# Kernel tuning notes

Measured on AMD Instinct MI355X. Metric: run time of the kernel, lower is better.

## Reference

```python
import jax, jax.numpy as jnp
import numpy as np
from jax import lax

K = 3      # kernel size
PAD = 1    # padding (stride=1, dilation=1, single offset group)


def _deform_conv2d(x, off, weight, bias):
    # x: [B,C,H,W], off: [B,2*K*K,H,W] (y,x per tap), weight: [O,C,K,K], bias: [O]
    B, C, H, W = x.shape
    KK = K * K
    off = off.reshape(B, KK, 2, H, W)
    off_y, off_x = off[:, :, 0], off[:, :, 1]          # [B,KK,H,W]

    kh = jnp.repeat(jnp.arange(K, dtype=x.dtype), K)   # [KK] tap row offsets
    kw = jnp.tile(jnp.arange(K, dtype=x.dtype), K)     # [KK] tap col offsets
    py = (jnp.arange(H, dtype=x.dtype)[None, None, :, None] - PAD
          + kh[None, :, None, None] + off_y)           # [B,KK,H,W] sample rows
    px = (jnp.arange(W, dtype=x.dtype)[None, None, None, :] - PAD
          + kw[None, :, None, None] + off_x)           # [B,KK,H,W] sample cols

    y0 = jnp.floor(py); x0 = jnp.floor(px)
    wy1 = py - y0; wx1 = px - x0
    wy0 = 1.0 - wy1; wx0 = 1.0 - wx1

    bidx = jnp.arange(B)[:, None, None, None]

    def gather(iy, ix):
        # zero outside the input (torchvision semantics)
        valid = (iy >= 0) & (iy < H) & (ix >= 0) & (ix < W)
        iyc = jnp.clip(iy, 0, H - 1).astype(jnp.int32)
        ixc = jnp.clip(ix, 0, W - 1).astype(jnp.int32)
        v = x[bidx, :, iyc, ixc]                       # [B,KK,H,W,C]
        return v * valid[..., None].astype(x.dtype)

    samp = (gather(y0, x0)           * (wy0 * wx0)[..., None]
            + gather(y0, x0 + 1)     * (wy0 * wx1)[..., None]
            + gather(y0 + 1, x0)     * (wy1 * wx0)[..., None]
            + gather(y0 + 1, x0 + 1) * (wy1 * wx1)[..., None])  # [B,KK,H,W,C]

    w = weight.reshape(weight.shape[0], C, KK)          # [O,C,KK]
    out = jnp.einsum('bkhwc,ock->bohw', samp, w) + bias[None, :, None, None]
    return out


def setup_inputs() -> dict:
    key = jax.random.key(0)
    k1, k2, k3 = jax.random.split(key, 3)
    B, C, O, H, W = 4, 64, 64, 128, 128
    x = jax.random.normal(k1, (B, C, H, W), dtype=jnp.float32)
    offset_w = jax.random.normal(k2, (2 * K * K, C, 3, 3), dtype=jnp.float32) * 0.02
    offset_b = jnp.zeros((2 * K * K,), dtype=jnp.float32)
    weight = jax.random.normal(k3, (O, C, K, K), dtype=jnp.float32) * 0.01
    bias = jnp.zeros((O,), dtype=jnp.float32)
    return {"x": x, "offset_w": offset_w, "offset_b": offset_b,
            "weight": weight, "bias": bias}


def reference(x, offset_w, offset_b, weight, bias):
    # offset-predicting conv (3x3, pad 1)
    off = lax.conv_general_dilated(
        x, offset_w, window_strides=(1, 1), padding='SAME',
        dimension_numbers=('NCHW', 'OIHW', 'NCHW')) + offset_b[None, :, None, None]
    return _deform_conv2d(x, off, weight, bias)
```

## Files before the change

kernel.cpp:

```cpp
#include <hip/hip_runtime.h>
#include <hip/hip_bf16.h>


typedef short short8 __attribute__((ext_vector_type(8)));
typedef short short4v __attribute__((ext_vector_type(4)));
typedef float f32x4 __attribute__((ext_vector_type(4)));

static __device__ inline short bf16s(float f) {
    __hip_bfloat16 h = __float2bfloat16(f);
    return *(short*)&h;
}
static __device__ inline float lo2f(unsigned u) { return __uint_as_float(u << 16); }
static __device__ inline float hi2f(unsigned u) { return __uint_as_float(u & 0xffff0000u); }

__global__ void prep_kernel(const float* __restrict__ offset_w,
                            const float* __restrict__ weight,
                            __hip_bfloat16* __restrict__ Wb,
                            __hip_bfloat16* __restrict__ OWb)
{
    int id = blockIdx.x * 256 + threadIdx.x;
    if (id < 36864) {
        int j    = id & 7;
        int lane = (id >> 3) & 63;
        int id3  = id >> 9;
        int s    = id3 % 18;
        int otile = id3 / 18;
        int n = lane & 15, q = lane >> 4;
        int kap = s * 32 + q * 8 + j;
        int k = kap >> 6, c = kap & 63;
        int o = otile * 16 + n;
        Wb[id] = __float2bfloat16(weight[(o * 64 + c) * 9 + k]);
    }
    int id2 = id - 36864;
    if (id2 >= 0 && id2 < 18432) {
        int j    = id2 & 7;
        int lane = (id2 >> 3) & 63;
        int id3  = id2 >> 9;
        int s    = id3 % 18;
        int ntile = id3 / 18;
        int n = lane & 15, q = lane >> 4;
        int kap = s * 32 + q * 8 + j;
        int k = kap >> 6, c = kap & 63;
        int o = ntile * 16 + n;
        float v = (o < 18) ? offset_w[(o * 64 + c) * 9 + k] : 0.0f;
        OWb[id2] = __float2bfloat16(v);
    }
}

__global__ void transpose_kernel(const float* __restrict__ x, __hip_bfloat16* __restrict__ xB)
{
    __shared__ __align__(16) float lds[128 * 65];
    int bh = blockIdx.x;
    int b = bh >> 7, h = bh & 127;
    int t = threadIdx.x;
    int w = t & 127, chalf = t >> 7;
    for (int i = 0; i < 32; ++i) {
        int c = i * 2 + chalf;
        lds[w * 65 + c] = x[((b * 64 + c) * 128 + h) * 128 + w];
    }
    __syncthreads();
    unsigned* dst = (unsigned*)(xB + ((b * 128 + h) * 128) * 64);
    for (int i = 0; i < 16; ++i) {
        int L = i * 256 + t;
        int ww = L >> 5, c2 = L & 31;
        float f0 = lds[ww * 65 + c2 * 2];
        float f1 = lds[ww * 65 + c2 * 2 + 1];
        unsigned pk = ((unsigned)bf16s(f0) & 0xffffu) | ((unsigned)bf16s(f1) << 16);
        dst[L] = pk;
    }
}

__global__ __launch_bounds__(256, 6) void deform_kernel(
    const __hip_bfloat16* __restrict__ xB,
    const __hip_bfloat16* __restrict__ Wb,
    const __hip_bfloat16* __restrict__ OWb,
    const float* __restrict__ offset_b,
    const float* __restrict__ bias,
    float* __restrict__ out)
{
    __shared__ __align__(16) short sampB[18 * 16 * 40];
    __shared__ __align__(16) float offL[288];

    int t = threadIdx.x, wv = t >> 6, lane = t & 63;
    int bid = blockIdx.x;
    int b  = bid >> 10;
    int h  = (bid >> 3) & 127;
    int w0 = (bid & 7) << 4;

    short* patch = sampB;

    {
        int c2 = t & 31, pg = t >> 5;
        const __hip_bfloat16* xbb = xB + b * (128 * 128 * 64) + c2 * 2;
#pragma unroll
        for (int i = 0; i < 7; ++i) {
            int pix = i * 8 + pg;
            if (pix < 54) {
                int row = pix / 18, col = pix - row * 18;
                int hh = h - 1 + row, ww2 = w0 - 1 + col;
                unsigned v = 0;
                if (hh >= 0 && hh < 128 && ww2 >= 0 && ww2 < 128)
                    v = *(const unsigned*)(xbb + (hh * 128 + ww2) * 64);
                *(unsigned*)&patch[pix * 80 + c2 * 2] = v;
            }
        }
    }
    __syncthreads();

    if (wv < 2) {
        int n = lane & 15, q = lane >> 4;
        const short8* Bw = (const short8*)OWb + (wv * 18) * 64 + lane;
        f32x4 acc = {0.f, 0.f, 0.f, 0.f};
#pragma unroll
        for (int s = 0; s < 18; ++s) {
            int k = s >> 1;
            int ky = k / 3, kx = k - ky * 3;
            int pix = ky * 18 + n + kx;
            const short8 a = *(const short8*)&patch[pix * 80 + (s & 1) * 32 + q * 8];
            acc = __builtin_amdgcn_mfma_f32_16x16x32_bf16(a, Bw[s * 64], acc, 0, 0, 0);
        }
        int o = wv * 16 + n;
        if (o < 18) {
            float bo = offset_b[o];
#pragma unroll
            for (int r = 0; r < 4; ++r)
                offL[o * 16 + q * 4 + r] = acc[r] + bo;
        }
    }
    __syncthreads();

    {
        int g = lane >> 4, c4 = lane & 15;
        int p = wv * 4 + g;
        const __hip_bfloat16* xb4 = xB + b * (128 * 128 * 64) + c4 * 4;

        float offy[9], offx[9];
#pragma unroll
        for (int k = 0; k < 9; ++k) {
            offy[k] = offL[(2 * k) * 16 + p];
            offx[k] = offL[(2 * k + 1) * 16 + p];
        }

#pragma unroll
        for (int k = 0; k < 9; ++k) {
            float py = (float)(h - 1 + (k / 3)) + offy[k];
            float px = (float)(w0 + p - 1 + (k % 3)) + offx[k];
            float y0f = floorf(py), x0f = floorf(px);
            float wy1 = py - y0f, wx1 = px - x0f;
            float wy0 = 1.0f - wy1, wx0 = 1.0f - wx1;
            int iy = (int)y0f, ix = (int)x0f;
            bool y0v = (iy >= 0) && (iy < 128);
            bool y1v = (iy >= -1) && (iy < 127);
            bool x0v = (ix >= 0) && (ix < 128);
            bool x1v = (ix >= -1) && (ix < 127);
            int iy0c = min(max(iy, 0), 127), iy1c = min(max(iy + 1, 0), 127);
            int ix0c = min(max(ix, 0), 127), ix1c = min(max(ix + 1, 0), 127);
            int e00 = (iy0c * 128 + ix0c) * 64;
            int e01 = (iy0c * 128 + ix1c) * 64;
            int e10 = (iy1c * 128 + ix0c) * 64;
            int e11 = (iy1c * 128 + ix1c) * 64;
            float wa = (y0v && x0v) ? wy0 * wx0 : 0.0f;
            float wb_ = (y0v && x1v) ? wy0 * wx1 : 0.0f;
            float wc = (y1v && x0v) ? wy1 * wx0 : 0.0f;
            float wd = (y1v && x1v) ? wy1 * wx1 : 0.0f;

            uint2 r0 = *(const uint2*)(xb4 + e00);
            uint2 r1 = *(const uint2*)(xb4 + e01);
            uint2 r2 = *(const uint2*)(xb4 + e10);
            uint2 r3 = *(const uint2*)(xb4 + e11);

            float s0 = fmaf(wd, lo2f(r3.x), fmaf(wc, lo2f(r2.x), fmaf(wb_, lo2f(r1.x), wa * lo2f(r0.x))));
            float s1 = fmaf(wd, hi2f(r3.x), fmaf(wc, hi2f(r2.x), fmaf(wb_, hi2f(r1.x), wa * hi2f(r0.x))));
            float s2 = fmaf(wd, lo2f(r3.y), fmaf(wc, lo2f(r2.y), fmaf(wb_, lo2f(r1.y), wa * lo2f(r0.y))));
            float s3 = fmaf(wd, hi2f(r3.y), fmaf(wc, hi2f(r2.y), fmaf(wb_, hi2f(r1.y), wa * hi2f(r0.y))));
            int s = 2 * k + (c4 >> 3);
            short4v pk = { bf16s(s0), bf16s(s1), bf16s(s2), bf16s(s3) };
            *(short4v*)&sampB[(s * 16 + p) * 40 + (c4 & 7) * 4] = pk;
        }
    }
    __syncthreads();

    {
        int n = lane & 15, q = lane >> 4;
        int arow = n * 40 + q * 8;
        const short8* BwW = (const short8*)Wb + (wv * 18) * 64 + lane;
        f32x4 acc = {0.f, 0.f, 0.f, 0.f};
#pragma unroll
        for (int s = 0; s < 18; ++s) {
            const short8 a = *(const short8*)&sampB[s * 640 + arow];
            acc = __builtin_amdgcn_mfma_f32_16x16x32_bf16(a, BwW[s * 64], acc, 0, 0, 0);
        }
        int o = wv * 16 + n;
        float bo = bias[o];
        float4 st = {acc[0] + bo, acc[1] + bo, acc[2] + bo, acc[3] + bo};
        *(float4*)&out[((b * 64 + o) * 128 + h) * 128 + w0 + q * 4] = st;
    }
}

extern "C" void kernel_launch(void* const* d_in, const int* in_sizes, int n_in,
                              void* d_out, int out_size, void* d_ws, size_t ws_size,
                              hipStream_t stream) {
    const float* x        = (const float*)d_in[0];
    const float* offset_w = (const float*)d_in[1];
    const float* offset_b = (const float*)d_in[2];
    const float* weight   = (const float*)d_in[3];
    const float* bias     = (const float*)d_in[4];
    char* ws = (char*)d_ws;
    __hip_bfloat16* xB  = (__hip_bfloat16*)ws;
    __hip_bfloat16* Wb  = (__hip_bfloat16*)(ws + 8388608);
    __hip_bfloat16* OWb = (__hip_bfloat16*)(ws + 8388608 + 73728);
    float* outp = (float*)d_out;

    hipLaunchKernelGGL(prep_kernel,      dim3(216),  dim3(256), 0, stream, offset_w, weight, Wb, OWb);
    hipLaunchKernelGGL(transpose_kernel, dim3(512),  dim3(256), 0, stream, x, xB);
    hipLaunchKernelGGL(deform_kernel,    dim3(4096), dim3(256), 0, stream, xB, Wb, OWb, offset_b, bias, outp);
}
```

Baseline: 115.1 us.

## Shrink deform tile to 8 pixels with 128 threads and XCD-aware block swizzle

Each deform block now covers 8 output pixels with two waves instead of 16 pixels with four waves. The grid doubles to 8192 blocks, and each wave computes two 16-channel output tiles with MFMA. Block IDs are remapped so that blocks scheduled on the same XCD handle a contiguous image region, which is meant to improve L2 reuse of the sampled input. In exchange, half of each 16-row MFMA A operand is duplicated or garbage rows that get discarded, and the 3-row input halo is loaded for only 8 pixels, so halo overhead per pixel rises.

```diff
diff --git a/kernel.cpp b/kernel.cpp
--- a/kernel.cpp
+++ b/kernel.cpp
@@ -70,7 +70,7 @@
     }
 }
 
-__global__ __launch_bounds__(256, 6) void deform_kernel(
+__global__ __launch_bounds__(128, 6) void deform_kernel(
     const __hip_bfloat16* __restrict__ xB,
     const __hip_bfloat16* __restrict__ Wb,
     const __hip_bfloat16* __restrict__ OWb,
@@ -78,36 +78,37 @@
     const float* __restrict__ bias,
     float* __restrict__ out)
 {
-    __shared__ __align__(16) short sampB[18 * 16 * 40];
-    __shared__ __align__(16) float offL[288];
+    __shared__ __align__(16) short sampB[18 * 8 * 40];
+    __shared__ __align__(16) float offL[18 * 8];
 
     int t = threadIdx.x, wv = t >> 6, lane = t & 63;
-    int bid = blockIdx.x;
-    int b  = bid >> 10;
-    int h  = (bid >> 3) & 127;
-    int w0 = (bid & 7) << 4;
+    int u = blockIdx.x;
+    int bid = (u & 7) * 1024 + (u >> 3);
+    int b  = bid >> 11;
+    int h  = (bid >> 4) & 127;
+    int w0 = (bid & 15) << 3;
 
     short* patch = sampB;
 
     {
-        int c2 = t & 31, pg = t >> 5;
-        const __hip_bfloat16* xbb = xB + b * (128 * 128 * 64) + c2 * 2;
-#pragma unroll
-        for (int i = 0; i < 7; ++i) {
-            int pix = i * 8 + pg;
-            if (pix < 54) {
-                int row = pix / 18, col = pix - row * 18;
+        const __hip_bfloat16* xbb = xB + b * (128 * 128 * 64);
+#pragma unroll
+        for (int i = 0; i < 8; ++i) {
+            int idx = i * 128 + t;
+            if (idx < 960) {
+                int c2 = idx & 31, pix = idx >> 5;
+                int row = pix / 10, col = pix - row * 10;
                 int hh = h - 1 + row, ww2 = w0 - 1 + col;
                 unsigned v = 0;
                 if (hh >= 0 && hh < 128 && ww2 >= 0 && ww2 < 128)
-                    v = *(const unsigned*)(xbb + (hh * 128 + ww2) * 64);
+                    v = *(const unsigned*)(xbb + (hh * 128 + ww2) * 64 + c2 * 2);
                 *(unsigned*)&patch[pix * 80 + c2 * 2] = v;
             }
         }
     }
     __syncthreads();
 
-    if (wv < 2) {
+    {
         int n = lane & 15, q = lane >> 4;
         const short8* Bw = (const short8*)OWb + (wv * 18) * 64 + lane;
         f32x4 acc = {0.f, 0.f, 0.f, 0.f};
@@ -115,16 +116,16 @@
         for (int s = 0; s < 18; ++s) {
             int k = s >> 1;
             int ky = k / 3, kx = k - ky * 3;
-            int pix = ky * 18 + n + kx;
+            int pix = ky * 10 + n + kx;
             const short8 a = *(const short8*)&patch[pix * 80 + (s & 1) * 32 + q * 8];
             acc = __builtin_amdgcn_mfma_f32_16x16x32_bf16(a, Bw[s * 64], acc, 0, 0, 0);
         }
         int o = wv * 16 + n;
-        if (o < 18) {
+        if (o < 18 && q < 2) {
             float bo = offset_b[o];
 #pragma unroll
             for (int r = 0; r < 4; ++r)
-                offL[o * 16 + q * 4 + r] = acc[r] + bo;
+                offL[o * 8 + q * 4 + r] = acc[r] + bo;
         }
     }
     __syncthreads();
@@ -137,8 +138,8 @@
         float offy[9], offx[9];
 #pragma unroll
         for (int k = 0; k < 9; ++k) {
-            offy[k] = offL[(2 * k) * 16 + p];
-            offx[k] = offL[(2 * k + 1) * 16 + p];
+            offy[k] = offL[(2 * k) * 8 + p];
+            offx[k] = offL[(2 * k + 1) * 8 + p];
         }
 
 #pragma unroll
@@ -159,10 +160,10 @@
             int e01 = (iy0c * 128 + ix1c) * 64;
             int e10 = (iy1c * 128 + ix0c) * 64;
             int e11 = (iy1c * 128 + ix1c) * 64;
-            float wa = (y0v && x0v) ? wy0 * wx0 : 0.0f;
+            float wa  = (y0v && x0v) ? wy0 * wx0 : 0.0f;
             float wb_ = (y0v && x1v) ? wy0 * wx1 : 0.0f;
-            float wc = (y1v && x0v) ? wy1 * wx0 : 0.0f;
-            float wd = (y1v && x1v) ? wy1 * wx1 : 0.0f;
+            float wc  = (y1v && x0v) ? wy1 * wx0 : 0.0f;
+            float wd  = (y1v && x1v) ? wy1 * wx1 : 0.0f;
 
             uint2 r0 = *(const uint2*)(xb4 + e00);
             uint2 r1 = *(const uint2*)(xb4 + e01);
@@ -175,25 +176,33 @@
             float s3 = fmaf(wd, hi2f(r3.y), fmaf(wc, hi2f(r2.y), fmaf(wb_, hi2f(r1.y), wa * hi2f(r0.y))));
             int s = 2 * k + (c4 >> 3);
             short4v pk = { bf16s(s0), bf16s(s1), bf16s(s2), bf16s(s3) };
-            *(short4v*)&sampB[(s * 16 + p) * 40 + (c4 & 7) * 4] = pk;
-        }
-    }
-    __syncthreads();
-
-    {
-        int n = lane & 15, q = lane >> 4;
-        int arow = n * 40 + q * 8;
-        const short8* BwW = (const short8*)Wb + (wv * 18) * 64 + lane;
-        f32x4 acc = {0.f, 0.f, 0.f, 0.f};
+            *(short4v*)&sampB[(s * 8 + p) * 40 + (c4 & 7) * 4] = pk;
+        }
+    }
+    __syncthreads();
+
+    {
+        int n = lane & 15, q = lane >> 4;
+        int arow = (n & 7) * 40 + q * 8;
+        const short8* Bw0 = (const short8*)Wb + ((wv * 2 + 0) * 18) * 64 + lane;
+        const short8* Bw1 = (const short8*)Wb + ((wv * 2 + 1) * 18) * 64 + lane;
+        f32x4 acc0 = {0.f, 0.f, 0.f, 0.f};
+        f32x4 acc1 = {0.f, 0.f, 0.f, 0.f};
 #pragma unroll
         for (int s = 0; s < 18; ++s) {
-            const short8 a = *(const short8*)&sampB[s * 640 + arow];
-            acc = __builtin_amdgcn_mfma_f32_16x16x32_bf16(a, BwW[s * 64], acc, 0, 0, 0);
-        }
-        int o = wv * 16 + n;
-        float bo = bias[o];
-        float4 st = {acc[0] + bo, acc[1] + bo, acc[2] + bo, acc[3] + bo};
-        *(float4*)&out[((b * 64 + o) * 128 + h) * 128 + w0 + q * 4] = st;
+            const short8 a = *(const short8*)&sampB[s * 320 + arow];
+            acc0 = __builtin_amdgcn_mfma_f32_16x16x32_bf16(a, Bw0[s * 64], acc0, 0, 0, 0);
+            acc1 = __builtin_amdgcn_mfma_f32_16x16x32_bf16(a, Bw1[s * 64], acc1, 0, 0, 0);
+        }
+        if (q < 2) {
+            int o0 = (wv * 2 + 0) * 16 + n;
+            int o1 = (wv * 2 + 1) * 16 + n;
+            float b0 = bias[o0], b1 = bias[o1];
+            float4 st0 = {acc0[0] + b0, acc0[1] + b0, acc0[2] + b0, acc0[3] + b0};
+            float4 st1 = {acc1[0] + b1, acc1[1] + b1, acc1[2] + b1, acc1[3] + b1};
+            *(float4*)&out[((b * 64 + o0) * 128 + h) * 128 + w0 + q * 4] = st0;
+            *(float4*)&out[((b * 64 + o1) * 128 + h) * 128 + w0 + q * 4] = st1;
+        }
     }
 }
 
@@ -213,5 +222,5 @@
 
     hipLaunchKernelGGL(prep_kernel,      dim3(216),  dim3(256), 0, stream, offset_w, weight, Wb, OWb);
     hipLaunchKernelGGL(transpose_kernel, dim3(512),  dim3(256), 0, stream, x, xB);
-    hipLaunchKernelGGL(deform_kernel,    dim3(4096), dim3(256), 0, stream, xB, Wb, OWb, offset_b, bias, outp);
-}
+    hipLaunchKernelGGL(deform_kernel,    dim3(8192), dim3(128), 0, stream, xB, Wb, OWb, offset_b, bias, outp);
+}
```

Result: slower. 129.5 us (+12.5%).

## Collapse deform kernel to one wave per tile with register-resident sampled operands

Applied to the files above, without the earlier changes.

The deform kernel now uses a single 64-lane wave per 16-pixel tile instead of four waves. The wave builds the bilinear-sampled A fragments directly in registers, laid out for the MFMA, and feeds them straight into four output-tile accumulators, removing the LDS sample buffer and two block barriers. The offset conv also reads its inputs straight from global memory instead of staging a halo patch in LDS. In exchange, each wave does four times the interpolation and MFMA work, register pressure rises, and per-block parallelism drops, so latency hiding depends on many more resident waves.

```diff
diff --git a/kernel.cpp b/kernel.cpp
--- a/kernel.cpp
+++ b/kernel.cpp
@@ -3,7 +3,6 @@
 
 
 typedef short short8 __attribute__((ext_vector_type(8)));
-typedef short short4v __attribute__((ext_vector_type(4)));
 typedef float f32x4 __attribute__((ext_vector_type(4)));
 
 static __device__ inline short bf16s(float f) {
@@ -70,7 +69,7 @@
     }
 }
 
-__global__ __launch_bounds__(256, 6) void deform_kernel(
+__global__ __launch_bounds__(64, 4) void deform_kernel(
     const __hip_bfloat16* __restrict__ xB,
     const __hip_bfloat16* __restrict__ Wb,
     const __hip_bfloat16* __restrict__ OWb,
@@ -78,73 +77,63 @@
     const float* __restrict__ bias,
     float* __restrict__ out)
 {
-    __shared__ __align__(16) short sampB[18 * 16 * 40];
     __shared__ __align__(16) float offL[288];
 
-    int t = threadIdx.x, wv = t >> 6, lane = t & 63;
+    int lane = threadIdx.x;
+    int n = lane & 15, q = lane >> 4;
     int bid = blockIdx.x;
     int b  = bid >> 10;
     int h  = (bid >> 3) & 127;
     int w0 = (bid & 7) << 4;
 
-    short* patch = sampB;
+    const __hip_bfloat16* xbb = xB + b * (128 * 128 * 64);
 
     {
-        int c2 = t & 31, pg = t >> 5;
-        const __hip_bfloat16* xbb = xB + b * (128 * 128 * 64) + c2 * 2;
-#pragma unroll
-        for (int i = 0; i < 7; ++i) {
-            int pix = i * 8 + pg;
-            if (pix < 54) {
-                int row = pix / 18, col = pix - row * 18;
-                int hh = h - 1 + row, ww2 = w0 - 1 + col;
-                unsigned v = 0;
-                if (hh >= 0 && hh < 128 && ww2 >= 0 && ww2 < 128)
-                    v = *(const unsigned*)(xbb + (hh * 128 + ww2) * 64);
-                *(unsigned*)&patch[pix * 80 + c2 * 2] = v;
-            }
-        }
-    }
-    __syncthreads();
-
-    if (wv < 2) {
-        int n = lane & 15, q = lane >> 4;
-        const short8* Bw = (const short8*)OWb + (wv * 18) * 64 + lane;
-        f32x4 acc = {0.f, 0.f, 0.f, 0.f};
+        const short8* B0 = (const short8*)OWb + lane;
+        f32x4 acc0 = {0.f, 0.f, 0.f, 0.f};
+        f32x4 acc1 = {0.f, 0.f, 0.f, 0.f};
 #pragma unroll
         for (int s = 0; s < 18; ++s) {
             int k = s >> 1;
             int ky = k / 3, kx = k - ky * 3;
-            int pix = ky * 18 + n + kx;
-            const short8 a = *(const short8*)&patch[pix * 80 + (s & 1) * 32 + q * 8];
-            acc = __builtin_amdgcn_mfma_f32_16x16x32_bf16(a, Bw[s * 64], acc, 0, 0, 0);
+            int hh = h - 1 + ky, ww = w0 + n - 1 + kx;
+            bool ok = (hh >= 0) && (hh < 128) && (ww >= 0) && (ww < 128);
+            int hhc = min(max(hh, 0), 127), wwc = min(max(ww, 0), 127);
+            uint4 av = *(const uint4*)(xbb + (hhc * 128 + wwc) * 64 + (s & 1) * 32 + q * 8);
+            if (!ok) { av.x = 0; av.y = 0; av.z = 0; av.w = 0; }
+            short8 a = *(short8*)&av;
+            acc0 = __builtin_amdgcn_mfma_f32_16x16x32_bf16(a, B0[(0 * 18 + s) * 64], acc0, 0, 0, 0);
+            acc1 = __builtin_amdgcn_mfma_f32_16x16x32_bf16(a, B0[(1 * 18 + s) * 64], acc1, 0, 0, 0);
         }
-        int o = wv * 16 + n;
-        if (o < 18) {
-            float bo = offset_b[o];
+        float bo0 = offset_b[n];
+#pragma unroll
+        for (int r = 0; r < 4; ++r)
+            offL[n * 16 + q * 4 + r] = acc0[r] + bo0;
+        if (n < 2) {
+            float bo1 = offset_b[16 + n];
 #pragma unroll
             for (int r = 0; r < 4; ++r)
-                offL[o * 16 + q * 4 + r] = acc[r] + bo;
+                offL[(16 + n) * 16 + q * 4 + r] = acc1[r] + bo1;
         }
     }
     __syncthreads();
 
+    float offy[9], offx[9];
+#pragma unroll
+    for (int k = 0; k < 9; ++k) {
+        offy[k] = offL[(2 * k) * 16 + n];
+        offx[k] = offL[(2 * k + 1) * 16 + n];
+    }
+
+    f32x4 acc[4] = { {0.f,0.f,0.f,0.f}, {0.f,0.f,0.f,0.f}, {0.f,0.f,0.f,0.f}, {0.f,0.f,0.f,0.f} };
     {
-        int g = lane >> 4, c4 = lane & 15;
-        int p = wv * 4 + g;
-        const __hip_bfloat16* xb4 = xB + b * (128 * 128 * 64) + c4 * 4;
-
-        float offy[9], offx[9];
-#pragma unroll
-        for (int k = 0; k < 9; ++k) {
-            offy[k] = offL[(2 * k) * 16 + p];
-            offx[k] = offL[(2 * k + 1) * 16 + p];
-        }
-
+        const short8* BwL = (const short8*)Wb + lane;
+        const __hip_bfloat16* xA = xbb + q * 8;
+        const __hip_bfloat16* xBc = xbb + 32 + q * 8;
 #pragma unroll
         for (int k = 0; k < 9; ++k) {
             float py = (float)(h - 1 + (k / 3)) + offy[k];
-            float px = (float)(w0 + p - 1 + (k % 3)) + offx[k];
+            float px = (float)(w0 + n - 1 + (k % 3)) + offx[k];
             float y0f = floorf(py), x0f = floorf(px);
             float wy1 = py - y0f, wx1 = px - x0f;
             float wy0 = 1.0f - wy1, wx0 = 1.0f - wx1;
@@ -159,40 +148,62 @@
             int e01 = (iy0c * 128 + ix1c) * 64;
             int e10 = (iy1c * 128 + ix0c) * 64;
             int e11 = (iy1c * 128 + ix1c) * 64;
-            float wa = (y0v && x0v) ? wy0 * wx0 : 0.0f;
+            float wa  = (y0v && x0v) ? wy0 * wx0 : 0.0f;
             float wb_ = (y0v && x1v) ? wy0 * wx1 : 0.0f;
-            float wc = (y1v && x0v) ? wy1 * wx0 : 0.0f;
-            float wd = (y1v && x1v) ? wy1 * wx1 : 0.0f;
-
-            uint2 r0 = *(const uint2*)(xb4 + e00);
-            uint2 r1 = *(const uint2*)(xb4 + e01);
-            uint2 r2 = *(const uint2*)(xb4 + e10);
-            uint2 r3 = *(const uint2*)(xb4 + e11);
-
-            float s0 = fmaf(wd, lo2f(r3.x), fmaf(wc, lo2f(r2.x), fmaf(wb_, lo2f(r1.x), wa * lo2f(r0.x))));
-            float s1 = fmaf(wd, hi2f(r3.x), fmaf(wc, hi2f(r2.x), fmaf(wb_, hi2f(r1.x), wa * hi2f(r0.x))));
-            float s2 = fmaf(wd, lo2f(r3.y), fmaf(wc, lo2f(r2.y), fmaf(wb_, lo2f(r1.y), wa * lo2f(r0.y))));
-            float s3 = fmaf(wd, hi2f(r3.y), fmaf(wc, hi2f(r2.y), fmaf(wb_, hi2f(r1.y), wa * hi2f(r0.y))));
-            int s = 2 * k + (c4 >> 3);
-            short4v pk = { bf16s(s0), bf16s(s1), bf16s(s2), bf16s(s3) };
-            *(short4v*)&sampB[(s * 16 + p) * 40 + (c4 & 7) * 4] = pk;
+            float wc  = (y1v && x0v) ? wy1 * wx0 : 0.0f;
+            float wd  = (y1v && x1v) ? wy1 * wx1 : 0.0f;
+
+            uint4 A0 = *(const uint4*)(xA + e00);
+            uint4 A1 = *(const uint4*)(xA + e01);
+            uint4 A2 = *(const uint4*)(xA + e10);
+            uint4 A3 = *(const uint4*)(xA + e11);
+            uint4 C0 = *(const uint4*)(xBc + e00);
+            uint4 C1 = *(const uint4*)(xBc + e01);
+            uint4 C2 = *(const uint4*)(xBc + e10);
+            uint4 C3 = *(const uint4*)(xBc + e11);
+
+            short8 a0, a1;
+            {
+                const unsigned* u0 = (const unsigned*)&A0;
+                const unsigned* u1 = (const unsigned*)&A1;
+                const unsigned* u2 = (const unsigned*)&A2;
+                const unsigned* u3 = (const unsigned*)&A3;
+#pragma unroll
+                for (int c2 = 0; c2 < 4; ++c2) {
+                    float lo = fmaf(wd, lo2f(u3[c2]), fmaf(wc, lo2f(u2[c2]), fmaf(wb_, lo2f(u1[c2]), wa * lo2f(u0[c2]))));
+                    float hi = fmaf(wd, hi2f(u3[c2]), fmaf(wc, hi2f(u2[c2]), fmaf(wb_, hi2f(u1[c2]), wa * hi2f(u0[c2]))));
+                    a0[c2 * 2]     = bf16s(lo);
+                    a0[c2 * 2 + 1] = bf16s(hi);
+                }
+            }
+            {
+                const unsigned* u0 = (const unsigned*)&C0;
+                const unsigned* u1 = (const unsigned*)&C1;
+                const unsigned* u2 = (const unsigned*)&C2;
+                const unsigned* u3 = (const unsigned*)&C3;
+#pragma unroll
+                for (int c2 = 0; c2 < 4; ++c2) {
+                    float lo = fmaf(wd, lo2f(u3[c2]), fmaf(wc, lo2f(u2[c2]), fmaf(wb_, lo2f(u1[c2]), wa * lo2f(u0[c2]))));
+                    float hi = fmaf(wd, hi2f(u3[c2]), fmaf(wc, hi2f(u2[c2]), fmaf(wb_, hi2f(u1[c2]), wa * hi2f(u0[c2]))));
+                    a1[c2 * 2]     = bf16s(lo);
+                    a1[c2 * 2 + 1] = bf16s(hi);
+                }
+            }
+
+            int s0 = 2 * k, s1 = 2 * k + 1;
+#pragma unroll
+            for (int ot = 0; ot < 4; ++ot) {
+                acc[ot] = __builtin_amdgcn_mfma_f32_16x16x32_bf16(a0, BwL[(ot * 18 + s0) * 64], acc[ot], 0, 0, 0);
+                acc[ot] = __builtin_amdgcn_mfma_f32_16x16x32_bf16(a1, BwL[(ot * 18 + s1) * 64], acc[ot], 0, 0, 0);
+            }
         }
     }
-    __syncthreads();
-
-    {
-        int n = lane & 15, q = lane >> 4;
-        int arow = n * 40 + q * 8;
-        const short8* BwW = (const short8*)Wb + (wv * 18) * 64 + lane;
-        f32x4 acc = {0.f, 0.f, 0.f, 0.f};
-#pragma unroll
-        for (int s = 0; s < 18; ++s) {
-            const short8 a = *(const short8*)&sampB[s * 640 + arow];
-            acc = __builtin_amdgcn_mfma_f32_16x16x32_bf16(a, BwW[s * 64], acc, 0, 0, 0);
-        }
-        int o = wv * 16 + n;
+
+#pragma unroll
+    for (int ot = 0; ot < 4; ++ot) {
+        int o = ot * 16 + n;
         float bo = bias[o];
-        float4 st = {acc[0] + bo, acc[1] + bo, acc[2] + bo, acc[3] + bo};
+        float4 st = {acc[ot][0] + bo, acc[ot][1] + bo, acc[ot][2] + bo, acc[ot][3] + bo};
         *(float4*)&out[((b * 64 + o) * 128 + h) * 128 + w0 + q * 4] = st;
     }
 }
@@ -213,5 +224,5 @@
 
     hipLaunchKernelGGL(prep_kernel,      dim3(216),  dim3(256), 0, stream, offset_w, weight, Wb, OWb);
     hipLaunchKernelGGL(transpose_kernel, dim3(512),  dim3(256), 0, stream, x, xB);
-    hipLaunchKernelGGL(deform_kernel,    dim3(4096), dim3(256), 0, stream, xB, Wb, OWb, offset_b, bias, outp);
-}
+    hipLaunchKernelGGL(deform_kernel,    dim3(4096), dim3(64),  0, stream, xB, Wb, OWb, offset_b, bias, outp);
+}
```

Measured after the change: 130.1 us. +13.0%, slower.
